# Kernel tuning notes

Measured on AMD Instinct MI355X. Metric: run time of the kernel, lower is better.

The kernel has to match this reference:

```python
import jax, jax.numpy as jnp
import numpy as np

GRID = 192          # grid_size (scaled up from the module's toy 32)
H = 0.1             # cell_size
VISC = 0.01         # viscosity
DT = 0.01           # config.time_step, passed as forward's dt
GRAV = 9.81


def setup_inputs() -> dict:
    key = jax.random.key(0)
    velocity_field = jax.random.normal(key, (3, GRID, GRID, GRID), dtype=jnp.float32)
    return {"velocity_field": velocity_field}


def _nb_sum(f):
    # 6-neighbor sum on the interior of the last three axes
    return (f[..., 2:, 1:-1, 1:-1] + f[..., :-2, 1:-1, 1:-1]
            + f[..., 1:-1, 2:, 1:-1] + f[..., 1:-1, :-2, 1:-1]
            + f[..., 1:-1, 1:-1, 2:] + f[..., 1:-1, 1:-1, :-2])


def _fluid_step(vel):
    N = GRID
    dt = DT
    # --- add_gravity ---
    vel = vel.at[2].add(-GRAV * dt)
    # --- advect: semi-Lagrangian backtrace + trilinear interpolation ---
    coords = jnp.arange(N, dtype=vel.dtype)
    X, Y, Z = jnp.meshgrid(coords, coords, coords, indexing='ij')
    pos = jnp.stack([X, Y, Z]) - vel * (dt / H)        # [3,N,N,N] backtraced positions
    pos = jnp.clip(pos, 0.0, float(N - 2))
    i0 = jnp.floor(pos).astype(jnp.int32)              # base corner, i1 = i0+1 <= N-1
    w1 = pos - i0.astype(vel.dtype)
    w0 = 1.0 - w1
    ix, iy, iz = i0[0], i0[1], i0[2]
    wx0, wy0, wz0 = w0[0], w0[1], w0[2]
    wx1, wy1, wz1 = w1[0], w1[1], w1[2]

    def g(di, dj, dk):
        return vel[:, ix + di, iy + dj, iz + dk]        # gather -> [3,N,N,N]

    vel = (g(0, 0, 0) * wx0 * wy0 * wz0 + g(0, 0, 1) * wx0 * wy0 * wz1
           + g(0, 1, 0) * wx0 * wy1 * wz0 + g(0, 1, 1) * wx0 * wy1 * wz1
           + g(1, 0, 0) * wx1 * wy0 * wz0 + g(1, 0, 1) * wx1 * wy0 * wz1
           + g(1, 1, 0) * wx1 * wy1 * wz0 + g(1, 1, 1) * wx1 * wy1 * wz1)
    # --- diffuse: 5 Jacobi sweeps on the interior ---
    alpha = VISC * dt / (H * H)
    inv = 1.0 / (1.0 + 6.0 * alpha)
    for _ in range(5):
        interior = (vel[:, 1:-1, 1:-1, 1:-1] + alpha * _nb_sum(vel)) * inv
        vel = vel.at[:, 1:-1, 1:-1, 1:-1].set(interior)
    # --- project: central-difference divergence, 20 Jacobi pressure sweeps, gradient subtract ---
    div = jnp.zeros((N, N, N), vel.dtype)
    div_int = ((vel[0, 2:, 1:-1, 1:-1] - vel[0, :-2, 1:-1, 1:-1])
               + (vel[1, 1:-1, 2:, 1:-1] - vel[1, 1:-1, :-2, 1:-1])
               + (vel[2, 1:-1, 1:-1, 2:] - vel[2, 1:-1, 1:-1, :-2])) / (2.0 * H)
    div = div.at[1:-1, 1:-1, 1:-1].set(div_int)
    p = jnp.zeros_like(div)
    for _ in range(20):
        p = p.at[1:-1, 1:-1, 1:-1].set((div[1:-1, 1:-1, 1:-1] + _nb_sum(p)) / 6.0)
    inv2h = 1.0 / (2.0 * H)
    vel = vel.at[0, 1:-1, 1:-1, 1:-1].add(-(p[2:, 1:-1, 1:-1] - p[:-2, 1:-1, 1:-1]) * inv2h)
    vel = vel.at[1, 1:-1, 1:-1, 1:-1].add(-(p[1:-1, 2:, 1:-1] - p[1:-1, :-2, 1:-1]) * inv2h)
    vel = vel.at[2, 1:-1, 1:-1, 1:-1].add(-(p[1:-1, 1:-1, 2:] - p[1:-1, 1:-1, :-2]) * inv2h)
    return vel


def reference(velocity_field):
    return _fluid_step(velocity_field)
```

## Files before the change

kernel.cpp:

```cpp
#include <hip/hip_runtime.h>
#include <hip/hip_fp16.h>


constexpr int   N      = 192;
constexpr int   N2     = N * N;
constexpr int   N3     = N * N * N;
constexpr float GDT    = 9.81f * 0.01f;
constexpr float SCL    = 0.01f / 0.1f;
constexpr float ALPHA  = 0.01f * 0.01f / (0.1f * 0.1f);
constexpr float INVDIF = 1.0f / (1.0f + 6.0f * ALPHA);
constexpr float INV2H  = 1.0f / (2.0f * 0.1f);
constexpr float SIXTH  = 1.0f / 6.0f;

constexpr int NT4 = (N3 / 4) / 256;
constexpr int SLAB = NT4 / 8;

__device__ __forceinline__ int swz(int b) {
    return (b & 7) * SLAB + (b >> 3);
}

__device__ __forceinline__ void decomp(int id, int& i, int& j, int& k0) {
    i = id / N2;
    const int r = id - i * N2;
    j = r / N;
    k0 = r - j * N;
}

union H4u { ushort4 u; __half h[4]; };
__device__ __forceinline__ float4 ldh4(const __half* p) {
    H4u t; t.u = *(const ushort4*)p;
    return make_float4(__half2float(t.h[0]), __half2float(t.h[1]),
                       __half2float(t.h[2]), __half2float(t.h[3]));
}
__device__ __forceinline__ void sth4(__half* p, float x, float y, float z, float w) {
    H4u t;
    t.h[0] = __float2half(x); t.h[1] = __float2half(y);
    t.h[2] = __float2half(z); t.h[3] = __float2half(w);
    *(ushort4*)p = t.u;
}
__device__ __forceinline__ float ldh(const __half* p) { return __half2float(*p); }

constexpr int RS    = 196;
constexpr int TILEI = N / 2;
constexpr int TPS   = TILEI / 8;
constexpr int NBADV = (N / 2) * (N / 2);

__global__ __launch_bounds__(768) void k_advect(const float* __restrict__ vin,
                                                __half* __restrict__ vout) {
    __shared__ float s[48 * RS];

    const int lin = blockIdx.x;
    const int x   = lin & 7;
    const int q   = lin >> 3;
    const int il  = q % TPS;
    const int jt  = q / TPS;
    const int i0  = (x * TPS + il) * 2;
    const int j0  = jt * 2;

#pragma unroll
    for (int p = 0; p < 3; ++p) {
        const int f   = p * 768 + threadIdx.x;
        const int r   = f / 48;
        const int c4  = f - r * 48;
        const int c   = r >> 4;
        const int rem = r & 15;
        const int di  = rem >> 2;
        const int dj  = rem & 3;
        const int gi  = min(max(i0 + di - 1, 0), N - 1);
        const int gj  = min(max(j0 + dj - 1, 0), N - 1);
        *(float4*)&s[r * RS + c4 * 4] =
            *(const float4*)&vin[c * N3 + gi * N2 + gj * N + c4 * 4];
    }
    __syncthreads();

    const int t  = threadIdx.x / 192;
    const int k  = threadIdx.x - t * 192;
    const int li = t >> 1;
    const int lj = t & 1;
    const int i  = i0 + li;
    const int j  = j0 + lj;
    const int id = (i * N + j) * N + k;

    const int cr = ((li + 1) * 4 + (lj + 1)) * RS + k;
    const float vx = s[cr];
    const float vy = s[16 * RS + cr];
    const float vz = s[32 * RS + cr] - GDT;

    float px = (float)i - vx * SCL;
    float py = (float)j - vy * SCL;
    float pz = (float)k - vz * SCL;
    const float hi = (float)(N - 2);
    px = fminf(fmaxf(px, 0.0f), hi);
    py = fminf(fmaxf(py, 0.0f), hi);
    pz = fminf(fmaxf(pz, 0.0f), hi);

    const int ix = (int)px;
    const int iy = (int)py;
    const int iz = (int)pz;

    float g[3][8];
    const bool in = (ix >= i - 1) & (ix <= i) & (iy >= j - 1) & (iy <= j);
    if (in) {
        const int lix = ix - i0 + 1;
        const int liy = iy - j0 + 1;
#pragma unroll
        for (int c = 0; c < 3; ++c) {
            const int r00 = ((c * 16 + lix * 4 + liy)) * RS + iz;
            const int r01 = r00 + RS;
            const int r10 = r00 + 4 * RS;
            const int r11 = r10 + RS;
            g[c][0] = s[r00];     g[c][1] = s[r00 + 1];
            g[c][2] = s[r01];     g[c][3] = s[r01 + 1];
            g[c][4] = s[r10];     g[c][5] = s[r10 + 1];
            g[c][6] = s[r11];     g[c][7] = s[r11 + 1];
        }
    } else {
        const int base = (ix * N + iy) * N + iz;
#pragma unroll
        for (int c = 0; c < 3; ++c) {
            const float* f = vin + c * N3 + base;
            g[c][0] = f[0];      g[c][1] = f[1];
            g[c][2] = f[N];      g[c][3] = f[N + 1];
            g[c][4] = f[N2];     g[c][5] = f[N2 + 1];
            g[c][6] = f[N2 + N]; g[c][7] = f[N2 + N + 1];
        }
    }

    const float wx1 = px - (float)ix, wy1 = py - (float)iy, wz1 = pz - (float)iz;
    const float wx0 = 1.0f - wx1,     wy0 = 1.0f - wy1,     wz0 = 1.0f - wz1;
    const float w000 = wx0 * wy0 * wz0;
    const float w001 = wx0 * wy0 * wz1;
    const float w010 = wx0 * wy1 * wz0;
    const float w011 = wx0 * wy1 * wz1;
    const float w100 = wx1 * wy0 * wz0;
    const float w101 = wx1 * wy0 * wz1;
    const float w110 = wx1 * wy1 * wz0;
    const float w111 = wx1 * wy1 * wz1;

#pragma unroll
    for (int c = 0; c < 3; ++c) {
        float r = g[c][0] * w000 + g[c][1] * w001
                + g[c][2] * w010 + g[c][3] * w011
                + g[c][4] * w100 + g[c][5] * w101
                + g[c][6] * w110 + g[c][7] * w111;
        if (c == 2) r -= GDT;
        vout[c * N3 + id] = __float2half(r);
    }
}

__global__ __launch_bounds__(256) void k_diffh(const __half* __restrict__ vin,
                                               __half* __restrict__ vout) {
    const int gtid = swz(blockIdx.x) * 256 + threadIdx.x;
    const int id   = gtid << 2;
    int i, j, k0; decomp(id, i, j, k0);
    const int b = blockIdx.y * N3 + id;

    const float4 c = ldh4(vin + b);
    float4 out = c;
    if (i != 0 && i != N - 1 && j != 0 && j != N - 1) {
        const float4 ip = ldh4(vin + b + N2);
        const float4 im = ldh4(vin + b - N2);
        const float4 jp = ldh4(vin + b + N);
        const float4 jm = ldh4(vin + b - N);
        const float  km = (k0 > 0)     ? ldh(vin + b - 1) : 0.0f;
        const float  kp = (k0 < N - 4) ? ldh(vin + b + 4) : 0.0f;
        out.x = (c.x + ALPHA * (im.x + ip.x + jm.x + jp.x + km  + c.y)) * INVDIF;
        out.y = (c.y + ALPHA * (im.y + ip.y + jm.y + jp.y + c.x + c.z)) * INVDIF;
        out.z = (c.z + ALPHA * (im.z + ip.z + jm.z + jp.z + c.y + c.w)) * INVDIF;
        out.w = (c.w + ALPHA * (im.w + ip.w + jm.w + jp.w + c.z + kp )) * INVDIF;
        if (k0 == 0)     out.x = c.x;
        if (k0 == N - 4) out.w = c.w;
    }
    sth4(vout + b, out.x, out.y, out.z, out.w);
}

__global__ __launch_bounds__(256) void k_diffhf(const __half* __restrict__ vin,
                                                float* __restrict__ vout) {
    const int gtid = swz(blockIdx.x) * 256 + threadIdx.x;
    const int id   = gtid << 2;
    int i, j, k0; decomp(id, i, j, k0);
    const int b = blockIdx.y * N3 + id;

    const float4 c = ldh4(vin + b);
    float4 out = c;
    if (i != 0 && i != N - 1 && j != 0 && j != N - 1) {
        const float4 ip = ldh4(vin + b + N2);
        const float4 im = ldh4(vin + b - N2);
        const float4 jp = ldh4(vin + b + N);
        const float4 jm = ldh4(vin + b - N);
        const float  km = (k0 > 0)     ? ldh(vin + b - 1) : 0.0f;
        const float  kp = (k0 < N - 4) ? ldh(vin + b + 4) : 0.0f;
        out.x = (c.x + ALPHA * (im.x + ip.x + jm.x + jp.x + km  + c.y)) * INVDIF;
        out.y = (c.y + ALPHA * (im.y + ip.y + jm.y + jp.y + c.x + c.z)) * INVDIF;
        out.z = (c.z + ALPHA * (im.z + ip.z + jm.z + jp.z + c.y + c.w)) * INVDIF;
        out.w = (c.w + ALPHA * (im.w + ip.w + jm.w + jp.w + c.z + kp )) * INVDIF;
        if (k0 == 0)     out.x = c.x;
        if (k0 == N - 4) out.w = c.w;
    }
    *(float4*)(vout + b) = out;
}

__global__ __launch_bounds__(256) void k_div4(const float* __restrict__ v,
                                              __half* __restrict__ dv) {
    const int gtid = swz(blockIdx.x) * 256 + threadIdx.x;
    const int id   = gtid << 2;
    int i, j, k0; decomp(id, i, j, k0);

    float ox = 0.f, oy = 0.f, oz = 0.f, ow = 0.f;
    if (i != 0 && i != N - 1 && j != 0 && j != N - 1) {
        const float4 xp = *(const float4*)(v + id + N2);
        const float4 xm = *(const float4*)(v + id - N2);
        const float4 yp = *(const float4*)(v + N3 + id + N);
        const float4 ym = *(const float4*)(v + N3 + id - N);
        const float4 z  = *(const float4*)(v + 2 * N3 + id);
        const float  zm = (k0 > 0)     ? v[2 * N3 + id - 1] : 0.0f;
        const float  zp = (k0 < N - 4) ? v[2 * N3 + id + 4] : 0.0f;
        ox = ((xp.x - xm.x) + (yp.x - ym.x) + (z.y - zm )) * INV2H;
        oy = ((xp.y - xm.y) + (yp.y - ym.y) + (z.z - z.x)) * INV2H;
        oz = ((xp.z - xm.z) + (yp.z - ym.z) + (z.w - z.y)) * INV2H;
        ow = ((xp.w - xm.w) + (yp.w - ym.w) + (zp  - z.z)) * INV2H;
        if (k0 == 0)     ox = 0.f;
        if (k0 == N - 4) ow = 0.f;
    }
    sth4(dv + id, ox, oy, oz, ow);
}

__global__ __launch_bounds__(256) void k_p2_4(const __half* __restrict__ dv,
                                              __half* __restrict__ p) {
    const int gtid = swz(blockIdx.x) * 256 + threadIdx.x;
    const int id   = gtid << 2;
    int i, j, k0; decomp(id, i, j, k0);

    float ox = 0.f, oy = 0.f, oz = 0.f, ow = 0.f;
    if (i != 0 && i != N - 1 && j != 0 && j != N - 1) {
        const float4 c  = ldh4(dv + id);
        const float4 ip = ldh4(dv + id + N2);
        const float4 im = ldh4(dv + id - N2);
        const float4 jp = ldh4(dv + id + N);
        const float4 jm = ldh4(dv + id - N);
        const float  km = (k0 > 0)     ? ldh(dv + id - 1) : 0.0f;
        const float  kp = (k0 < N - 4) ? ldh(dv + id + 4) : 0.0f;
        ox = (c.x + (im.x + ip.x + jm.x + jp.x + km  + c.y) * SIXTH) * SIXTH;
        oy = (c.y + (im.y + ip.y + jm.y + jp.y + c.x + c.z) * SIXTH) * SIXTH;
        oz = (c.z + (im.z + ip.z + jm.z + jp.z + c.y + c.w) * SIXTH) * SIXTH;
        ow = (c.w + (im.w + ip.w + jm.w + jp.w + c.z + kp ) * SIXTH) * SIXTH;
        if (k0 == 0)     ox = 0.f;
        if (k0 == N - 4) ow = 0.f;
    }
    sth4(p + id, ox, oy, oz, ow);
}

__global__ __launch_bounds__(256) void k_jacobi4(const __half* __restrict__ pin,
                                                 const __half* __restrict__ dv,
                                                 __half* __restrict__ pout) {
    const int gtid = swz(blockIdx.x) * 256 + threadIdx.x;
    const int id   = gtid << 2;
    int i, j, k0; decomp(id, i, j, k0);

    float ox = 0.f, oy = 0.f, oz = 0.f, ow = 0.f;
    if (i != 0 && i != N - 1 && j != 0 && j != N - 1) {
        const float4 c  = ldh4(pin + id);
        const float4 ip = ldh4(pin + id + N2);
        const float4 im = ldh4(pin + id - N2);
        const float4 jp = ldh4(pin + id + N);
        const float4 jm = ldh4(pin + id - N);
        const float4 d  = ldh4(dv + id);
        const float  km = (k0 > 0)     ? ldh(pin + id - 1) : 0.0f;
        const float  kp = (k0 < N - 4) ? ldh(pin + id + 4) : 0.0f;
        ox = (d.x + im.x + ip.x + jm.x + jp.x + km  + c.y) * SIXTH;
        oy = (d.y + im.y + ip.y + jm.y + jp.y + c.x + c.z) * SIXTH;
        oz = (d.z + im.z + ip.z + jm.z + jp.z + c.y + c.w) * SIXTH;
        ow = (d.w + im.w + ip.w + jm.w + jp.w + c.z + kp ) * SIXTH;
        if (k0 == 0)     ox = 0.f;
        if (k0 == N - 4) ow = 0.f;
    }
    sth4(pout + id, ox, oy, oz, ow);
}

__global__ __launch_bounds__(256) void k_grad4(float* __restrict__ vel,
                                               const __half* __restrict__ p) {
    const int gtid = swz(blockIdx.x) * 256 + threadIdx.x;
    const int id   = gtid << 2;
    int i, j, k0; decomp(id, i, j, k0);
    if (i == 0 || i == N - 1 || j == 0 || j == N - 1) return;

    const float4 xp = ldh4(p + id + N2);
    const float4 xm = ldh4(p + id - N2);
    const float4 yp = ldh4(p + id + N);
    const float4 ym = ldh4(p + id - N);
    const float4 c  = ldh4(p + id);
    const float  pm = (k0 > 0)     ? ldh(p + id - 1) : 0.0f;
    const float  pp = (k0 < N - 4) ? ldh(p + id + 4) : 0.0f;

    const bool bx = (k0 == 0);
    const bool bw = (k0 == N - 4);

    float4 v0 = *(float4*)(vel + id);
    if (!bx) v0.x -= (xp.x - xm.x) * INV2H;
             v0.y -= (xp.y - xm.y) * INV2H;
             v0.z -= (xp.z - xm.z) * INV2H;
    if (!bw) v0.w -= (xp.w - xm.w) * INV2H;
    *(float4*)(vel + id) = v0;

    float4 v1 = *(float4*)(vel + N3 + id);
    if (!bx) v1.x -= (yp.x - ym.x) * INV2H;
             v1.y -= (yp.y - ym.y) * INV2H;
             v1.z -= (yp.z - ym.z) * INV2H;
    if (!bw) v1.w -= (yp.w - ym.w) * INV2H;
    *(float4*)(vel + N3 + id) = v1;

    float4 v2 = *(float4*)(vel + 2 * N3 + id);
    if (!bx) v2.x -= (c.y - pm ) * INV2H;
             v2.y -= (c.z - c.x) * INV2H;
             v2.z -= (c.w - c.y) * INV2H;
    if (!bw) v2.w -= (pp  - c.z) * INV2H;
    *(float4*)(vel + 2 * N3 + id) = v2;
}

extern "C" void kernel_launch(void* const* d_in, const int* in_sizes, int n_in,
                              void* d_out, int out_size, void* d_ws, size_t ws_size,
                              hipStream_t stream) {
    const float* vin  = (const float*)d_in[0];
    float*       vout = (float*)d_out;

    __half* hws  = (__half*)d_ws;
    __half* velA = hws;
    __half* velB = hws + 3 * N3;
    __half* dv   = hws;
    __half* pA   = hws + N3;
    __half* pB   = hws + 2 * N3;

    const dim3 blkA(768, 1, 1);
    const dim3 gridA(NBADV, 1, 1);
    const dim3 blk4(256, 1, 1);
    const dim3 grid4_1(NT4, 1, 1);
    const dim3 grid4_3(NT4, 3, 1);

    k_advect<<<gridA, blkA, 0, stream>>>(vin, velA);

    k_diffh <<<grid4_3, blk4, 0, stream>>>(velA, velB);
    k_diffh <<<grid4_3, blk4, 0, stream>>>(velB, velA);
    k_diffh <<<grid4_3, blk4, 0, stream>>>(velA, velB);
    k_diffh <<<grid4_3, blk4, 0, stream>>>(velB, velA);
    k_diffhf<<<grid4_3, blk4, 0, stream>>>(velA, vout);

    k_div4<<<grid4_1, blk4, 0, stream>>>(vout, dv);
    k_p2_4<<<grid4_1, blk4, 0, stream>>>(dv, pA);
    __half* pin  = pA;
    __half* pout = pB;
    for (int s = 0; s < 18; ++s) {
        k_jacobi4<<<grid4_1, blk4, 0, stream>>>(pin, dv, pout);
        __half* t = pin; pin = pout; pout = t;
    }
    k_grad4<<<grid4_1, blk4, 0, stream>>>(vout, pin);
}
```

Before: 518.2 us.

## Fuse pairs of Jacobi sweeps into one kernel via shared-memory halo tiles

Adds temporally-blocked kernels that each load a 4x4 column tile with a 2-cell halo into LDS, compute an intermediate sweep on a 6x6 region, then the second sweep on the 4x4 interior. Pressure Jacobi launches drop from 18 to 9 and the first four diffusion sweeps from four launches to two, halving global memory round-trips for those sweeps. In exchange it adds redundant halo loads and halo computation, large LDS use per block (about 52 KB), and scalar 16-bit stores in place of vectorized ones.

```diff
diff --git a/kernel.cpp b/kernel.cpp
--- a/kernel.cpp
+++ b/kernel.cpp
@@ -39,6 +39,9 @@
     *(ushort4*)p = t.u;
 }
 __device__ __forceinline__ float ldh(const __half* p) { return __half2float(*p); }
+__device__ __forceinline__ float h2f(ushort u) {
+    __half_raw r; r.x = u; return __half2float(__half(r));
+}
 
 constexpr int RS    = 196;
 constexpr int TILEI = N / 2;
@@ -148,8 +151,154 @@
     }
 }
 
-__global__ __launch_bounds__(256) void k_diffh(const __half* __restrict__ vin,
-                                               __half* __restrict__ vout) {
+constexpr int NPT = N / 4;
+constexpr int NBP = NPT * NPT;
+constexpr int PTS = NPT / 8;
+
+__global__ __launch_bounds__(768) void k_jacobi2(const __half* __restrict__ pin,
+                                                 const __half* __restrict__ dv,
+                                                 __half* __restrict__ pout) {
+    __shared__ ushort sp[64][192];
+    __shared__ float  sq[36][192];
+
+    const int lin = blockIdx.x;
+    const int x   = lin & 7;
+    const int qq  = lin >> 3;
+    const int il  = qq % PTS;
+    const int jt  = qq / PTS;
+    const int i0  = (x * PTS + il) * 4;
+    const int j0  = jt * 4;
+
+#pragma unroll
+    for (int p = 0; p < 4; ++p) {
+        const int f  = p * 768 + threadIdx.x;
+        const int r  = f / 48;
+        const int c4 = f - r * 48;
+        const int di = r >> 3;
+        const int dj = r & 7;
+        const int gi = min(max(i0 - 2 + di, 0), N - 1);
+        const int gj = min(max(j0 - 2 + dj, 0), N - 1);
+        *(ushort4*)&sp[r][c4 * 4] =
+            *(const ushort4*)((const ushort*)pin + (gi * N + gj) * N + c4 * 4);
+    }
+    __syncthreads();
+
+    const int g = threadIdx.x / 192;
+    const int k = threadIdx.x - g * 192;
+
+#pragma unroll
+    for (int rr = 0; rr < 9; ++rr) {
+        const int r  = rr * 4 + g;
+        const int di = r / 6;
+        const int dj = r - di * 6;
+        const int gi = i0 - 1 + di;
+        const int gj = j0 - 1 + dj;
+        float q = 0.0f;
+        if (gi >= 1 && gi <= N - 2 && gj >= 1 && gj <= N - 2 && k >= 1 && k <= N - 2) {
+            const int sr = (di + 1) * 8 + (dj + 1);
+            const float d = ldh(dv + (gi * N + gj) * N + k);
+            const float s = h2f(sp[sr - 8][k]) + h2f(sp[sr + 8][k])
+                          + h2f(sp[sr - 1][k]) + h2f(sp[sr + 1][k])
+                          + h2f(sp[sr][k - 1]) + h2f(sp[sr][k + 1]);
+            q = (d + s) * SIXTH;
+        }
+        sq[r][k] = q;
+    }
+    __syncthreads();
+
+#pragma unroll
+    for (int rr = 0; rr < 4; ++rr) {
+        const int r  = rr * 4 + g;
+        const int li = r >> 2;
+        const int lj = r & 3;
+        const int gi = i0 + li;
+        const int gj = j0 + lj;
+        float o = 0.0f;
+        if (gi >= 1 && gi <= N - 2 && gj >= 1 && gj <= N - 2 && k >= 1 && k <= N - 2) {
+            const int qr = (li + 1) * 6 + (lj + 1);
+            const float d = ldh(dv + (gi * N + gj) * N + k);
+            const float s = sq[qr - 6][k] + sq[qr + 6][k]
+                          + sq[qr - 1][k] + sq[qr + 1][k]
+                          + sq[qr][k - 1] + sq[qr][k + 1];
+            o = (d + s) * SIXTH;
+        }
+        ((__half*)pout)[(gi * N + gj) * N + k] = __float2half(o);
+    }
+}
+
+__global__ __launch_bounds__(768) void k_diffh2(const __half* __restrict__ vin,
+                                                __half* __restrict__ vout) {
+    __shared__ ushort sp[64][192];
+    __shared__ float  sq[36][192];
+
+    const int cb  = blockIdx.y * N3;
+    const int lin = blockIdx.x;
+    const int x   = lin & 7;
+    const int qq  = lin >> 3;
+    const int il  = qq % PTS;
+    const int jt  = qq / PTS;
+    const int i0  = (x * PTS + il) * 4;
+    const int j0  = jt * 4;
+
+#pragma unroll
+    for (int p = 0; p < 4; ++p) {
+        const int f  = p * 768 + threadIdx.x;
+        const int r  = f / 48;
+        const int c4 = f - r * 48;
+        const int di = r >> 3;
+        const int dj = r & 7;
+        const int gi = min(max(i0 - 2 + di, 0), N - 1);
+        const int gj = min(max(j0 - 2 + dj, 0), N - 1);
+        *(ushort4*)&sp[r][c4 * 4] =
+            *(const ushort4*)((const ushort*)vin + cb + (gi * N + gj) * N + c4 * 4);
+    }
+    __syncthreads();
+
+    const int g = threadIdx.x / 192;
+    const int k = threadIdx.x - g * 192;
+
+#pragma unroll
+    for (int rr = 0; rr < 9; ++rr) {
+        const int r  = rr * 4 + g;
+        const int di = r / 6;
+        const int dj = r - di * 6;
+        const int gi = i0 - 1 + di;
+        const int gj = j0 - 1 + dj;
+        const int sr = (di + 1) * 8 + (dj + 1);
+        const float c = h2f(sp[sr][k]);
+        float q = c;
+        if (gi >= 1 && gi <= N - 2 && gj >= 1 && gj <= N - 2 && k >= 1 && k <= N - 2) {
+            const float s = h2f(sp[sr - 8][k]) + h2f(sp[sr + 8][k])
+                          + h2f(sp[sr - 1][k]) + h2f(sp[sr + 1][k])
+                          + h2f(sp[sr][k - 1]) + h2f(sp[sr][k + 1]);
+            q = (c + ALPHA * s) * INVDIF;
+        }
+        sq[r][k] = q;
+    }
+    __syncthreads();
+
+#pragma unroll
+    for (int rr = 0; rr < 4; ++rr) {
+        const int r  = rr * 4 + g;
+        const int li = r >> 2;
+        const int lj = r & 3;
+        const int gi = i0 + li;
+        const int gj = j0 + lj;
+        const int qr = (li + 1) * 6 + (lj + 1);
+        const float c = sq[qr][k];
+        float o = c;
+        if (gi >= 1 && gi <= N - 2 && gj >= 1 && gj <= N - 2 && k >= 1 && k <= N - 2) {
+            const float s = sq[qr - 6][k] + sq[qr + 6][k]
+                          + sq[qr - 1][k] + sq[qr + 1][k]
+                          + sq[qr][k - 1] + sq[qr][k + 1];
+            o = (c + ALPHA * s) * INVDIF;
+        }
+        vout[cb + (gi * N + gj) * N + k] = __float2half(o);
+    }
+}
+
+__global__ __launch_bounds__(256) void k_diffhf(const __half* __restrict__ vin,
+                                                float* __restrict__ vout) {
     const int gtid = swz(blockIdx.x) * 256 + threadIdx.x;
     const int id   = gtid << 2;
     int i, j, k0; decomp(id, i, j, k0);
@@ -171,32 +320,6 @@
         if (k0 == 0)     out.x = c.x;
         if (k0 == N - 4) out.w = c.w;
     }
-    sth4(vout + b, out.x, out.y, out.z, out.w);
-}
-
-__global__ __launch_bounds__(256) void k_diffhf(const __half* __restrict__ vin,
-                                                float* __restrict__ vout) {
-    const int gtid = swz(blockIdx.x) * 256 + threadIdx.x;
-    const int id   = gtid << 2;
-    int i, j, k0; decomp(id, i, j, k0);
-    const int b = blockIdx.y * N3 + id;
-
-    const float4 c = ldh4(vin + b);
-    float4 out = c;
-    if (i != 0 && i != N - 1 && j != 0 && j != N - 1) {
-        const float4 ip = ldh4(vin + b + N2);
-        const float4 im = ldh4(vin + b - N2);
-        const float4 jp = ldh4(vin + b + N);
-        const float4 jm = ldh4(vin + b - N);
-        const float  km = (k0 > 0)     ? ldh(vin + b - 1) : 0.0f;
-        const float  kp = (k0 < N - 4) ? ldh(vin + b + 4) : 0.0f;
-        out.x = (c.x + ALPHA * (im.x + ip.x + jm.x + jp.x + km  + c.y)) * INVDIF;
-        out.y = (c.y + ALPHA * (im.y + ip.y + jm.y + jp.y + c.x + c.z)) * INVDIF;
-        out.z = (c.z + ALPHA * (im.z + ip.z + jm.z + jp.z + c.y + c.w)) * INVDIF;
-        out.w = (c.w + ALPHA * (im.w + ip.w + jm.w + jp.w + c.z + kp )) * INVDIF;
-        if (k0 == 0)     out.x = c.x;
-        if (k0 == N - 4) out.w = c.w;
-    }
     *(float4*)(vout + b) = out;
 }
 
@@ -250,33 +373,6 @@
     sth4(p + id, ox, oy, oz, ow);
 }
 
-__global__ __launch_bounds__(256) void k_jacobi4(const __half* __restrict__ pin,
-                                                 const __half* __restrict__ dv,
-                                                 __half* __restrict__ pout) {
-    const int gtid = swz(blockIdx.x) * 256 + threadIdx.x;
-    const int id   = gtid << 2;
-    int i, j, k0; decomp(id, i, j, k0);
-
-    float ox = 0.f, oy = 0.f, oz = 0.f, ow = 0.f;
-    if (i != 0 && i != N - 1 && j != 0 && j != N - 1) {
-        const float4 c  = ldh4(pin + id);
-        const float4 ip = ldh4(pin + id + N2);
-        const float4 im = ldh4(pin + id - N2);
-        const float4 jp = ldh4(pin + id + N);
-        const float4 jm = ldh4(pin + id - N);
-        const float4 d  = ldh4(dv + id);
-        const float  km = (k0 > 0)     ? ldh(pin + id - 1) : 0.0f;
-        const float  kp = (k0 < N - 4) ? ldh(pin + id + 4) : 0.0f;
-        ox = (d.x + im.x + ip.x + jm.x + jp.x + km  + c.y) * SIXTH;
-        oy = (d.y + im.y + ip.y + jm.y + jp.y + c.x + c.z) * SIXTH;
-        oz = (d.z + im.z + ip.z + jm.z + jp.z + c.y + c.w) * SIXTH;
-        ow = (d.w + im.w + ip.w + jm.w + jp.w + c.z + kp ) * SIXTH;
-        if (k0 == 0)     ox = 0.f;
-        if (k0 == N - 4) ow = 0.f;
-    }
-    sth4(pout + id, ox, oy, oz, ow);
-}
-
 __global__ __launch_bounds__(256) void k_grad4(float* __restrict__ vel,
                                                const __half* __restrict__ p) {
     const int gtid = swz(blockIdx.x) * 256 + threadIdx.x;
@@ -332,24 +428,25 @@
 
     const dim3 blkA(768, 1, 1);
     const dim3 gridA(NBADV, 1, 1);
+    const dim3 blkF(768, 1, 1);
+    const dim3 gridF1(NBP, 1, 1);
+    const dim3 gridF3(NBP, 3, 1);
     const dim3 blk4(256, 1, 1);
     const dim3 grid4_1(NT4, 1, 1);
     const dim3 grid4_3(NT4, 3, 1);
 
     k_advect<<<gridA, blkA, 0, stream>>>(vin, velA);
 
-    k_diffh <<<grid4_3, blk4, 0, stream>>>(velA, velB);
-    k_diffh <<<grid4_3, blk4, 0, stream>>>(velB, velA);
-    k_diffh <<<grid4_3, blk4, 0, stream>>>(velA, velB);
-    k_diffh <<<grid4_3, blk4, 0, stream>>>(velB, velA);
+    k_diffh2<<<gridF3, blkF, 0, stream>>>(velA, velB);
+    k_diffh2<<<gridF3, blkF, 0, stream>>>(velB, velA);
     k_diffhf<<<grid4_3, blk4, 0, stream>>>(velA, vout);
 
     k_div4<<<grid4_1, blk4, 0, stream>>>(vout, dv);
     k_p2_4<<<grid4_1, blk4, 0, stream>>>(dv, pA);
     __half* pin  = pA;
     __half* pout = pB;
-    for (int s = 0; s < 18; ++s) {
-        k_jacobi4<<<grid4_1, blk4, 0, stream>>>(pin, dv, pout);
+    for (int s = 0; s < 9; ++s) {
+        k_jacobi2<<<gridF1, blkF, 0, stream>>>(pin, dv, pout);
         __half* t = pin; pin = pout; pout = t;
     }
     k_grad4<<<grid4_1, blk4, 0, stream>>>(vout, pin);
```

Result: slower. 563.2 us (+8.7%).
